# Kernel tuning notes

Hardware: AMD Instinct MI355X
Metric: run time of the kernel (lower is better)

Reference implementation:

```python
import jax, jax.numpy as jnp
import numpy as np

B, T, D = 256, 512, 256

def setup_inputs() -> dict:
    key = jax.random.key(0)
    k1, k2, k3, k4 = jax.random.split(key, 4)
    ip = jax.random.normal(k1, (B, T, D), dtype=jnp.float32)
    W = jax.random.normal(k2, (D, D), dtype=jnp.float32) * (1.0 / np.sqrt(D))
    b = jax.random.normal(k3, (D,), dtype=jnp.float32) * 0.05
    context = jax.random.normal(k4, (D, 1), dtype=jnp.float32) * 0.05
    return {"ip": ip, "W": W, "b": b, "context": context}

def reference(ip, W, b, context) -> jnp.ndarray:
    # linear -> tanh: [B, T, D]
    h = jnp.tanh(jnp.einsum("btd,ed->bte", ip, W) + b)
    # attention scores over words: [B, T]
    scores = jnp.einsum("btd,d->bt", h, context[:, 0])
    attn = jax.nn.softmax(scores, axis=1)
    # weighted sum over words -> sentence embeddings: [B, D]
    sent_embeds = jnp.einsum("bt,btd->bd", attn, ip)
    return sent_embeds
```

## Files before the change

### kernel.cpp

```cpp
#include <hip/hip_runtime.h>
#include <hip/hip_bf16.h>

#define NBATCH 256
#define NT 512
#define ND 256

typedef __attribute__((ext_vector_type(8))) short short8;
typedef __attribute__((ext_vector_type(4))) float floatx4;

__device__ __forceinline__ unsigned short f2bf(float x) {
    unsigned int u = __float_as_uint(x);
    u += 0x7FFFu + ((u >> 16) & 1u);
    return (unsigned short)(u >> 16);
}

__global__ void __launch_bounds__(256) prep_kernel(
    const float* __restrict__ W, unsigned short* __restrict__ wbf)
{
    int i = (blockIdx.x * 256 + threadIdx.x) * 4;
    float4 f = *(const float4*)(W + i);
    ushort4 o;
    o.x = f2bf(f.x); o.y = f2bf(f.y); o.z = f2bf(f.z); o.w = f2bf(f.w);
    *(ushort4*)(wbf + i) = o;
}

__global__ void __launch_bounds__(1024) fused_kernel(
    const float* __restrict__ ip,
    const unsigned short* __restrict__ wbf,
    const float* __restrict__ bias,
    const float* __restrict__ ctx,
    float* __restrict__ out)
{
    __shared__ __align__(16) char wsm[32768];
    __shared__ float sc_buf[NT];
    __shared__ float attn_s[NT];
    __shared__ float red[16];
    __shared__ float bias_s[ND];
    __shared__ float ctx_s[ND];

    const int tid  = threadIdx.x;
    const int lane = tid & 63;
    const int wv   = tid >> 6;
    const int m    = lane & 15;
    const int q    = lane >> 4;
    const int b    = blockIdx.x;
    const long row0 = (long)b * NT + wv * 32;

    if (tid < ND) { bias_s[tid] = bias[tid]; ctx_s[tid] = ctx[tid]; }

    short8 a[2][8];
#pragma unroll
    for (int tile = 0; tile < 2; ++tile) {
        const float* ar = ip + (row0 + tile * 16 + m) * ND + q * 8;
#pragma unroll
        for (int s = 0; s < 8; ++s) {
            float4 f0 = *(const float4*)(ar + s * 32);
            float4 f1 = *(const float4*)(ar + s * 32 + 4);
            short8 v;
            v[0] = (short)f2bf(f0.x); v[1] = (short)f2bf(f0.y);
            v[2] = (short)f2bf(f0.z); v[3] = (short)f2bf(f0.w);
            v[4] = (short)f2bf(f1.x); v[5] = (short)f2bf(f1.y);
            v[6] = (short)f2bf(f1.z); v[7] = (short)f2bf(f1.w);
            a[tile][s] = v;
        }
    }

    float sc0[4] = {0.f, 0.f, 0.f, 0.f};
    float sc1[4] = {0.f, 0.f, 0.f, 0.f};
    const short8* wch = (const short8*)wbf;

#pragma unroll 1
    for (int stage = 0; stage < 4; ++stage) {
        if (stage) __syncthreads();
#pragma unroll
        for (int u = 0; u < 2; ++u) {
            int c  = stage * 2048 + tid + u * 1024;
            int cm = c & 15, cq = (c >> 4) & 3, cs = (c >> 6) & 7, cnb = c >> 9;
            int G  = ((cnb * 16 + cm) << 5) + cq + (cs << 2);
            *(short8*)(wsm + ((tid + u * 1024) << 4)) = wch[G];
        }
        __syncthreads();

#pragma unroll 1
        for (int nbl = 0; nbl < 4; ++nbl) {
            const int nb = stage * 4 + nbl;
            const int e  = nb * 16 + m;
            const char* wbase = wsm + (((nbl << 9) + lane) << 4);
            short8 w[8];
#pragma unroll
            for (int s = 0; s < 8; ++s)
                w[s] = *(const short8*)(wbase + (s << 10));
            floatx4 acc0 = {0.f, 0.f, 0.f, 0.f};
            floatx4 acc1 = {0.f, 0.f, 0.f, 0.f};
#pragma unroll
            for (int s = 0; s < 8; ++s) {
                acc0 = __builtin_amdgcn_mfma_f32_16x16x32_bf16(a[0][s], w[s], acc0, 0, 0, 0);
                acc1 = __builtin_amdgcn_mfma_f32_16x16x32_bf16(a[1][s], w[s], acc1, 0, 0, 0);
            }
            const float be = bias_s[e];
            const float ce = ctx_s[e];
#pragma unroll
            for (int r = 0; r < 4; ++r) {
                float x0 = acc0[r] + be;
                float x1 = acc1[r] + be;
                sc0[r] += (1.f - 2.f / (__expf(2.f * x0) + 1.f)) * ce;
                sc1[r] += (1.f - 2.f / (__expf(2.f * x1) + 1.f)) * ce;
            }
        }
    }

#pragma unroll
    for (int off = 8; off >= 1; off >>= 1) {
#pragma unroll
        for (int r = 0; r < 4; ++r) {
            sc0[r] += __shfl_xor(sc0[r], off, 64);
            sc1[r] += __shfl_xor(sc1[r], off, 64);
        }
    }
    if (m == 0) {
#pragma unroll
        for (int r = 0; r < 4; ++r) {
            sc_buf[wv * 32 + q * 4 + r]      = sc0[r];
            sc_buf[wv * 32 + 16 + q * 4 + r] = sc1[r];
        }
    }
    __syncthreads();

    float s = 0.f;
    if (tid < NT) {
        s = sc_buf[tid];
        float mx = s;
#pragma unroll
        for (int off = 32; off >= 1; off >>= 1) mx = fmaxf(mx, __shfl_xor(mx, off, 64));
        if (lane == 0) red[wv] = mx;
    }
    __syncthreads();
    float mx = red[0];
#pragma unroll
    for (int i = 1; i < 8; ++i) mx = fmaxf(mx, red[i]);
    float ev = 0.f;
    if (tid < NT) {
        ev = __expf(s - mx);
        float sm = ev;
#pragma unroll
        for (int off = 32; off >= 1; off >>= 1) sm += __shfl_xor(sm, off, 64);
        if (lane == 0) red[8 + wv] = sm;
    }
    __syncthreads();
    float sum = 0.f;
#pragma unroll
    for (int i = 0; i < 8; ++i) sum += red[8 + i];
    if (tid < NT) attn_s[tid] = ev / sum;
    __syncthreads();

    float (*partial)[ND] = (float (*)[ND])wsm;
    const int dg = lane;
    const int ts = wv;
    const float4* base = (const float4*)(ip + (long)b * NT * ND) + dg;
    float a0 = 0.f, a1 = 0.f, a2 = 0.f, a3 = 0.f;
#pragma unroll 4
    for (int t = ts * 32; t < ts * 32 + 32; ++t) {
        float w = attn_s[t];
        float4 v = base[t * 64];
        a0 += w * v.x; a1 += w * v.y; a2 += w * v.z; a3 += w * v.w;
    }
    partial[ts][dg * 4 + 0] = a0;
    partial[ts][dg * 4 + 1] = a1;
    partial[ts][dg * 4 + 2] = a2;
    partial[ts][dg * 4 + 3] = a3;
    __syncthreads();
    if (tid < ND) {
        float r = 0.f;
#pragma unroll
        for (int i = 0; i < 16; ++i) r += partial[i][tid];
        out[(long)b * ND + tid] = r;
    }
}

extern "C" void kernel_launch(void* const* d_in, const int* in_sizes, int n_in,
                              void* d_out, int out_size, void* d_ws, size_t ws_size,
                              hipStream_t stream) {
    const float* ip   = (const float*)d_in[0];
    const float* W    = (const float*)d_in[1];
    const float* bias = (const float*)d_in[2];
    const float* ctx  = (const float*)d_in[3];

    unsigned short* wbf = (unsigned short*)d_ws;

    prep_kernel<<<64, 256, 0, stream>>>(W, wbf);
    fused_kernel<<<NBATCH, 1024, 0, stream>>>(ip, wbf, bias, ctx, (float*)d_out);
}
```

Measured before the change: 250.8 us.

## Split fused kernel into scores GEMM kernel and softmax-weighted-sum kernel

Splits the single per-batch fused kernel into two kernels. The first computes tanh-linear scores for 128-row tiles using 256-thread blocks, and the second does the softmax and weighted sum split across four D-quarters per batch. The aim is more, smaller blocks for better occupancy and load balance. In exchange it adds a global round-trip for scores, a second pass over the input that may lose cache locality, and more reloading of W into LDS.

```diff
diff --git a/kernel.cpp b/kernel.cpp
--- a/kernel.cpp
+++ b/kernel.cpp
@@ -4,6 +4,7 @@
 #define NBATCH 256
 #define NT 512
 #define ND 256
+#define NROWS (NBATCH * NT)
 
 typedef __attribute__((ext_vector_type(8))) short short8;
 typedef __attribute__((ext_vector_type(4))) float floatx4;
@@ -24,17 +25,14 @@
     *(ushort4*)(wbf + i) = o;
 }
 
-__global__ void __launch_bounds__(1024) fused_kernel(
+__global__ void __launch_bounds__(256, 2) scores_kernel(
     const float* __restrict__ ip,
     const unsigned short* __restrict__ wbf,
     const float* __restrict__ bias,
     const float* __restrict__ ctx,
-    float* __restrict__ out)
+    float* __restrict__ scores)
 {
     __shared__ __align__(16) char wsm[32768];
-    __shared__ float sc_buf[NT];
-    __shared__ float attn_s[NT];
-    __shared__ float red[16];
     __shared__ float bias_s[ND];
     __shared__ float ctx_s[ND];
 
@@ -43,10 +41,10 @@
     const int wv   = tid >> 6;
     const int m    = lane & 15;
     const int q    = lane >> 4;
-    const int b    = blockIdx.x;
-    const long row0 = (long)b * NT + wv * 32;
+    const long row0 = (long)blockIdx.x * 128 + wv * 32;
 
-    if (tid < ND) { bias_s[tid] = bias[tid]; ctx_s[tid] = ctx[tid]; }
+    bias_s[tid] = bias[tid];
+    ctx_s[tid]  = ctx[tid];
 
     short8 a[2][8];
 #pragma unroll
@@ -73,18 +71,17 @@
     for (int stage = 0; stage < 4; ++stage) {
         if (stage) __syncthreads();
 #pragma unroll
-        for (int u = 0; u < 2; ++u) {
-            int c  = stage * 2048 + tid + u * 1024;
+        for (int u = 0; u < 8; ++u) {
+            int c  = stage * 2048 + tid + u * 256;
             int cm = c & 15, cq = (c >> 4) & 3, cs = (c >> 6) & 7, cnb = c >> 9;
             int G  = ((cnb * 16 + cm) << 5) + cq + (cs << 2);
-            *(short8*)(wsm + ((tid + u * 1024) << 4)) = wch[G];
+            *(short8*)(wsm + ((tid + u * 256) << 4)) = wch[G];
         }
         __syncthreads();
 
 #pragma unroll 1
         for (int nbl = 0; nbl < 4; ++nbl) {
-            const int nb = stage * 4 + nbl;
-            const int e  = nb * 16 + m;
+            const int e  = (stage * 4 + nbl) * 16 + m;
             const char* wbase = wsm + (((nbl << 9) + lane) << 4);
             short8 w[8];
 #pragma unroll
@@ -120,45 +117,53 @@
     if (m == 0) {
 #pragma unroll
         for (int r = 0; r < 4; ++r) {
-            sc_buf[wv * 32 + q * 4 + r]      = sc0[r];
-            sc_buf[wv * 32 + 16 + q * 4 + r] = sc1[r];
+            scores[row0 + q * 4 + r]      = sc0[r];
+            scores[row0 + 16 + q * 4 + r] = sc1[r];
         }
     }
+}
+
+__global__ void __launch_bounds__(256) wsum_kernel(
+    const float* __restrict__ ip,
+    const float* __restrict__ scores,
+    float* __restrict__ out)
+{
+    __shared__ float attn_s[NT];
+    __shared__ float red[8];
+    __shared__ float partial[16][64];
+
+    const int b  = blockIdx.x >> 2;
+    const int dq = blockIdx.x & 3;
+    const int tid  = threadIdx.x;
+    const int lane = tid & 63;
+    const int wv   = tid >> 6;
+
+    float s0 = scores[(long)b * NT + tid];
+    float s1 = scores[(long)b * NT + tid + 256];
+    float mx = fmaxf(s0, s1);
+#pragma unroll
+    for (int off = 32; off >= 1; off >>= 1) mx = fmaxf(mx, __shfl_xor(mx, off, 64));
+    if (lane == 0) red[wv] = mx;
+    __syncthreads();
+    mx = fmaxf(fmaxf(red[0], red[1]), fmaxf(red[2], red[3]));
+    float e0 = __expf(s0 - mx), e1 = __expf(s1 - mx);
+    float sm = e0 + e1;
+#pragma unroll
+    for (int off = 32; off >= 1; off >>= 1) sm += __shfl_xor(sm, off, 64);
+    __syncthreads();
+    if (lane == 0) red[4 + wv] = sm;
+    __syncthreads();
+    sm = red[4] + red[5] + red[6] + red[7];
+    float inv = 1.f / sm;
+    attn_s[tid]       = e0 * inv;
+    attn_s[tid + 256] = e1 * inv;
     __syncthreads();
 
-    float s = 0.f;
-    if (tid < NT) {
-        s = sc_buf[tid];
-        float mx = s;
-#pragma unroll
-        for (int off = 32; off >= 1; off >>= 1) mx = fmaxf(mx, __shfl_xor(mx, off, 64));
-        if (lane == 0) red[wv] = mx;
-    }
-    __syncthreads();
-    float mx = red[0];
-#pragma unroll
-    for (int i = 1; i < 8; ++i) mx = fmaxf(mx, red[i]);
-    float ev = 0.f;
-    if (tid < NT) {
-        ev = __expf(s - mx);
-        float sm = ev;
-#pragma unroll
-        for (int off = 32; off >= 1; off >>= 1) sm += __shfl_xor(sm, off, 64);
-        if (lane == 0) red[8 + wv] = sm;
-    }
-    __syncthreads();
-    float sum = 0.f;
-#pragma unroll
-    for (int i = 0; i < 8; ++i) sum += red[8 + i];
-    if (tid < NT) attn_s[tid] = ev / sum;
-    __syncthreads();
-
-    float (*partial)[ND] = (float (*)[ND])wsm;
-    const int dg = lane;
-    const int ts = wv;
-    const float4* base = (const float4*)(ip + (long)b * NT * ND) + dg;
+    const int dg = tid & 15;
+    const int ts = tid >> 4;
+    const float4* base = (const float4*)(ip + (long)b * NT * ND + dq * 64) + dg;
     float a0 = 0.f, a1 = 0.f, a2 = 0.f, a3 = 0.f;
-#pragma unroll 4
+#pragma unroll 8
     for (int t = ts * 32; t < ts * 32 + 32; ++t) {
         float w = attn_s[t];
         float4 v = base[t * 64];
@@ -169,11 +174,11 @@
     partial[ts][dg * 4 + 2] = a2;
     partial[ts][dg * 4 + 3] = a3;
     __syncthreads();
-    if (tid < ND) {
+    if (tid < 64) {
         float r = 0.f;
 #pragma unroll
         for (int i = 0; i < 16; ++i) r += partial[i][tid];
-        out[(long)b * ND + tid] = r;
+        out[(long)b * ND + dq * 64 + tid] = r;
     }
 }
 
@@ -186,7 +191,9 @@
     const float* ctx  = (const float*)d_in[3];
 
     unsigned short* wbf = (unsigned short*)d_ws;
+    float* scores = (float*)((char*)d_ws + ND * ND * sizeof(unsigned short));
 
     prep_kernel<<<64, 256, 0, stream>>>(W, wbf);
-    fused_kernel<<<NBATCH, 1024, 0, stream>>>(ip, wbf, bias, ctx, (float*)d_out);
+    scores_kernel<<<NROWS / 128, 256, 0, stream>>>(ip, wbf, bias, ctx, scores);
+    wsum_kernel<<<NBATCH * 4, 256, 0, stream>>>(ip, scores, (float*)d_out);
 }
```

After: 241.1 us. 1.04x faster.
